# Performance work log

Hardware: AMD Instinct MI355X
Metric: run time of the kernel (lower is better)

The kernel has to match this reference:

```python
import jax, jax.numpy as jnp
import numpy as np

N_NODES = 50000
N_EDGES = 800000
IN_CH = 64
OUT_CH = 64
NHEAD = 8


def _edge_softmax(e, dst, num_nodes):
    # segment softmax over incoming edges of each destination node,
    # elementwise over [H, D] feature dims (matches dgl edge_softmax)
    mx = jax.ops.segment_max(e, dst, num_segments=num_nodes)
    mx = jax.lax.stop_gradient(mx)
    ex = jnp.exp(e - mx[dst])
    s = jax.ops.segment_sum(ex, dst, num_segments=num_nodes)
    return ex / s[dst]


def setup_inputs() -> dict:
    key = jax.random.key(0)
    ks = jax.random.split(key, 10)
    ndata = jax.random.normal(ks[0], (N_NODES, IN_CH), dtype=jnp.float32)
    src = jax.random.randint(ks[1], (N_EDGES,), 0, N_NODES)
    dst = jax.random.randint(ks[2], (N_EDGES,), 0, N_NODES)
    sc = 1.0 / np.sqrt(IN_CH)
    W1 = jax.random.normal(ks[3], (IN_CH, OUT_CH), dtype=jnp.float32) * sc
    b1 = jnp.zeros((OUT_CH,), dtype=jnp.float32)
    W2 = jax.random.normal(ks[4], (IN_CH, OUT_CH), dtype=jnp.float32) * sc
    b2 = jnp.zeros((OUT_CH,), dtype=jnp.float32)
    Wres = jax.random.normal(ks[5], (IN_CH, OUT_CH), dtype=jnp.float32) * sc
    bres = jnp.zeros((OUT_CH,), dtype=jnp.float32)
    m = jnp.ones((3, NHEAD, OUT_CH // NHEAD), dtype=jnp.float32)
    return {"ndata": ndata, "src": src, "dst": dst, "W1": W1, "b1": b1,
            "W2": W2, "b2": b2, "Wres": Wres, "bres": bres, "m": m}


def reference(ndata, src, dst, W1, b1, W2, b2, Wres, bres, m):
    N = ndata.shape[0]
    H = NHEAD
    # add self loops (dgl.add_self_loop)
    loop = jnp.arange(N, dtype=src.dtype)
    s = jnp.concatenate([src, loop])
    d = jnp.concatenate([dst, loop])
    # minmax_norm over last dim
    mn = jnp.min(ndata, axis=-1, keepdims=True)
    mx = jnp.max(ndata, axis=-1, keepdims=True)
    x = (ndata - mn) / (mx - mn + 1e-5)
    # node projections -> [N, H, Dh]
    l = (x @ W1 + b1).reshape(N, H, -1)
    r = (x @ W2 + b2).reshape(N, H, -1)
    # edge-wise fused activation of src+dst (acfun='sigmoid')
    le = jax.nn.sigmoid(l[s] + l[d])
    re = jax.nn.sigmoid(r[s] + r[d])
    # edge softmax grouped by destination
    le = _edge_softmax(le, d, N)
    re = _edge_softmax(re, d, N)
    # two-hop scatter-gather aggregation
    ft_r = jax.ops.segment_sum(r[s] * le, d, num_segments=N)   # [N,H,Dh]
    ft_l = jax.ops.segment_sum(ft_r[s] * re, d, num_segments=N)
    h = (m[0] * ft_l).reshape(N, -1) + (x @ Wres + bres)
    return h
```

## Files before the change

kernel.cpp:

```cpp
#include <hip/hip_runtime.h>
#include <hip/hip_fp16.h>

#define CH 64
#define LOG2E  1.44269504f
#define MLOG2E -1.44269504f

__device__ __forceinline__ float exp2fast(float x) {
    float r; asm("v_exp_f32 %0, %1" : "=v"(r) : "v"(x)); return r;
}

__global__ void count_kernel(const int* __restrict__ dst, int* __restrict__ deg,
                             int* __restrict__ rank, int E)
{
    for (int i = blockIdx.x * blockDim.x + threadIdx.x; i < E;
         i += gridDim.x * blockDim.x) {
        rank[i] = atomicAdd(&deg[dst[i]], 1);
    }
}

__global__ __launch_bounds__(256) void proj_kernel(
    const float* __restrict__ nd,
    const float* __restrict__ W1, const float* __restrict__ b1,
    const float* __restrict__ W2, const float* __restrict__ b2,
    const float* __restrict__ Wr, const float* __restrict__ br,
    __half2* __restrict__ lr, float* __restrict__ hres, int N)
{
    __shared__ __align__(16) float xs[4][CH];
    const int lane = threadIdx.x & 63;
    const int wid  = threadIdx.x >> 6;

    float w1[CH], w2[CH], wr[CH];
#pragma unroll
    for (int i = 0; i < CH; ++i) {
        w1[i] = W1[i * CH + lane];
        w2[i] = W2[i * CH + lane];
        wr[i] = Wr[i * CH + lane];
    }
    const float bb1 = b1[lane], bb2 = b2[lane], bbr = br[lane];

    const int nwave = gridDim.x * 4;
    for (int node = blockIdx.x * 4 + wid; node < N; node += nwave) {
        const unsigned row = (unsigned)node * CH;
        float v = nd[row + lane];
        float mn = v, mx = v;
#pragma unroll
        for (int off = 32; off; off >>= 1) {
            mn = fminf(mn, __shfl_xor(mn, off));
            mx = fmaxf(mx, __shfl_xor(mx, off));
        }
        float x = (v - mn) / (mx - mn + 1e-5f);
        xs[wid][lane] = x;
        float a1 = bb1, a2 = bb2, a3 = bbr;
        const float4* x4 = reinterpret_cast<const float4*>(&xs[wid][0]);
#pragma unroll
        for (int k = 0; k < CH / 4; ++k) {
            float4 xv = x4[k];
            a1 = fmaf(xv.x, w1[4*k+0], a1);
            a1 = fmaf(xv.y, w1[4*k+1], a1);
            a1 = fmaf(xv.z, w1[4*k+2], a1);
            a1 = fmaf(xv.w, w1[4*k+3], a1);
            a2 = fmaf(xv.x, w2[4*k+0], a2);
            a2 = fmaf(xv.y, w2[4*k+1], a2);
            a2 = fmaf(xv.z, w2[4*k+2], a2);
            a2 = fmaf(xv.w, w2[4*k+3], a2);
            a3 = fmaf(xv.x, wr[4*k+0], a3);
            a3 = fmaf(xv.y, wr[4*k+1], a3);
            a3 = fmaf(xv.z, wr[4*k+2], a3);
            a3 = fmaf(xv.w, wr[4*k+3], a3);
        }
        lr[row + lane]   = __floats2half2_rn(a1, a2);
        hres[row + lane] = a3;
    }
}

__global__ __launch_bounds__(256) void bsum_kernel(
    const int* __restrict__ deg, int* __restrict__ bsum, int N)
{
    __shared__ int ws[4];
    int i = blockIdx.x * 256 + threadIdx.x;
    int lane = threadIdx.x & 63, wid = threadIdx.x >> 6;
    int v = (i < N) ? deg[i] : 0;
#pragma unroll
    for (int off = 32; off; off >>= 1) v += __shfl_xor(v, off);
    if (lane == 0) ws[wid] = v;
    __syncthreads();
    if (threadIdx.x == 0) bsum[blockIdx.x] = ws[0] + ws[1] + ws[2] + ws[3];
}

__global__ __launch_bounds__(64) void bscan_kernel(int* __restrict__ bsum, int nb)
{
    int lane = threadIdx.x;
    int carry = 0;
    for (int base = 0; base < nb; base += 64) {
        int i = base + lane;
        int v = (i < nb) ? bsum[i] : 0;
        int s = v;
#pragma unroll
        for (int off = 1; off < 64; off <<= 1) {
            int t = __shfl_up(s, off);
            if (lane >= off) s += t;
        }
        if (i < nb) bsum[i] = carry + s - v;
        carry += __shfl(s, 63);
    }
}

__global__ __launch_bounds__(256) void apply_kernel(
    const int* __restrict__ deg, const int* __restrict__ bsum,
    int* __restrict__ rowptr, int N, int total)
{
    __shared__ int ws[4];
    int i = blockIdx.x * 256 + threadIdx.x;
    int lane = threadIdx.x & 63, wid = threadIdx.x >> 6;
    int v = (i < N) ? deg[i] : 0;
    int s = v;
#pragma unroll
    for (int off = 1; off < 64; off <<= 1) {
        int t = __shfl_up(s, off);
        if (lane >= off) s += t;
    }
    if (lane == 63) ws[wid] = s;
    __syncthreads();
    int woff = 0;
    for (int w = 0; w < wid; ++w) woff += ws[w];
    int excl = bsum[blockIdx.x] + woff + s - v;
    if (i < N) rowptr[i] = excl;
    if (blockIdx.x == 0 && threadIdx.x == 0) rowptr[N] = total;
}

__global__ void scatter_kernel(const int* __restrict__ src,
                               const int* __restrict__ dst,
                               const int* __restrict__ rank,
                               const int* __restrict__ rowptr,
                               int* __restrict__ col, int E)
{
    for (int i = blockIdx.x * blockDim.x + threadIdx.x; i < E;
         i += gridDim.x * blockDim.x) {
        col[rowptr[dst[i]] + rank[i]] = src[i];
    }
}

#define EDGE_BATCH(U_, TBL_, STEP_)                                          \
    {                                                                        \
        __half2 hb[U_];                                                      \
        _Pragma("unroll")                                                    \
        for (int u = 0; u < (U_); ++u) {                                     \
            int s_ = __builtin_amdgcn_readlane(myc, j + u);                  \
            hb[u] = TBL_[(unsigned)(s_ * CH) + lane];                        \
        }                                                                    \
        _Pragma("unroll")                                                    \
        for (int u = 0; u < (U_); ++u) { STEP_(hb[u]); }                     \
        j += (U_);                                                           \
    }

__global__ __launch_bounds__(256) void passA_kernel(
    const __half2* __restrict__ lr,
    const int* __restrict__ rowptr, const int* __restrict__ col,
    __half2* __restrict__ rf, int N)
{
    const int node = blockIdx.x * 4 + (threadIdx.x >> 6);
    const int lane = threadIdx.x & 63;
    if (node >= N) return;
    const unsigned row = (unsigned)node * CH;
    const float2 own = __half22float2(lr[row + lane]);
    const float l_d = own.x, r_d = own.y;
    const float nl_d = MLOG2E * l_d;
    const int beg = rowptr[node], end = rowptr[node + 1];

    float wl = exp2fast(LOG2E * __builtin_amdgcn_rcpf(1.f + exp2fast(2.f * nl_d)));
    float denL = wl, acc = r_d * wl;

#define A_STEP(H_) {                                                         \
        float2 f = __half22float2(H_);                                       \
        float uu = exp2fast(fmaf(f.x, MLOG2E, nl_d));                        \
        float w  = exp2fast(LOG2E * __builtin_amdgcn_rcpf(1.f + uu));        \
        denL += w; acc = fmaf(f.y, w, acc); }

    int e = beg;
    while (e < end) {
        int cnt = end - e; if (cnt > 64) cnt = 64;
        int idx = e + lane; if (idx >= end) idx = end - 1;
        const int myc = col[idx];
        int j = 0;
        int nfull = cnt >> 4;
        for (int b = 0; b < nfull; ++b) EDGE_BATCH(16, lr, A_STEP)
        if (cnt & 8) EDGE_BATCH(8, lr, A_STEP)
        if (cnt & 4) EDGE_BATCH(4, lr, A_STEP)
        if (cnt & 2) EDGE_BATCH(2, lr, A_STEP)
        if (cnt & 1) EDGE_BATCH(1, lr, A_STEP)
        e += cnt;
    }
    rf[row + lane] = __floats2half2_rn(r_d, acc / denL);
}

__global__ __launch_bounds__(256) void passB_kernel(
    const __half2* __restrict__ rf,
    const int* __restrict__ rowptr, const int* __restrict__ col,
    const float* __restrict__ m0, float* __restrict__ out, int N)
{
    const int node = blockIdx.x * 4 + (threadIdx.x >> 6);
    const int lane = threadIdx.x & 63;
    if (node >= N) return;
    const unsigned row = (unsigned)node * CH;
    const float2 own = __half22float2(rf[row + lane]);
    const float r_d = own.x, f_own = own.y;
    const float nr_d = MLOG2E * r_d;
    const int beg = rowptr[node], end = rowptr[node + 1];

    float wsl = exp2fast(LOG2E * __builtin_amdgcn_rcpf(1.f + exp2fast(2.f * nr_d)));
    float dR = wsl, acc = f_own * wsl;

#define B_STEP(H_) {                                                         \
        float2 f = __half22float2(H_);                                       \
        float uu = exp2fast(fmaf(f.x, MLOG2E, nr_d));                        \
        float w  = exp2fast(LOG2E * __builtin_amdgcn_rcpf(1.f + uu));        \
        dR += w; acc = fmaf(f.y, w, acc); }

    int e = beg;
    while (e < end) {
        int cnt = end - e; if (cnt > 64) cnt = 64;
        int idx = e + lane; if (idx >= end) idx = end - 1;
        const int myc = col[idx];
        int j = 0;
        int nfull = cnt >> 4;
        for (int b = 0; b < nfull; ++b) EDGE_BATCH(16, rf, B_STEP)
        if (cnt & 8) EDGE_BATCH(8, rf, B_STEP)
        if (cnt & 4) EDGE_BATCH(4, rf, B_STEP)
        if (cnt & 2) EDGE_BATCH(2, rf, B_STEP)
        if (cnt & 1) EDGE_BATCH(1, rf, B_STEP)
        e += cnt;
    }
    out[row + lane] = fmaf(m0[lane], acc / dR, out[row + lane]);
}

extern "C" void kernel_launch(void* const* d_in, const int* in_sizes, int n_in,
                              void* d_out, int out_size, void* d_ws, size_t ws_size,
                              hipStream_t stream)
{
    const float* ndata = (const float*)d_in[0];
    const int*   src   = (const int*)d_in[1];
    const int*   dst   = (const int*)d_in[2];
    const float* W1    = (const float*)d_in[3];
    const float* b1    = (const float*)d_in[4];
    const float* W2    = (const float*)d_in[5];
    const float* b2    = (const float*)d_in[6];
    const float* Wr    = (const float*)d_in[7];
    const float* br    = (const float*)d_in[8];
    const float* m     = (const float*)d_in[9];
    float* out = (float*)d_out;

    const int N = in_sizes[0] / CH;
    const int E = in_sizes[1];
    const int nbk = (N + 255) / 256;

    char* ws = (char*)d_ws;
    size_t off = 0;
    auto alloc = [&](size_t bytes) -> void* {
        void* p = ws + off;
        off = (off + bytes + 255) & ~(size_t)255;
        return p;
    };
    __half2* lr   = (__half2*)alloc((size_t)N * CH * 4);
    __half2* rf   = (__half2*)alloc((size_t)N * CH * 4);
    int*   deg    = (int*)alloc((size_t)N * 4);
    int*   bsum   = (int*)alloc((size_t)nbk * 4);
    int*   rowptr = (int*)alloc((size_t)(N + 1) * 4);
    int*   rank   = (int*)alloc((size_t)E * 4);
    int*   col    = (int*)alloc((size_t)E * 4);

    hipMemsetAsync(deg, 0, (size_t)N * 4, stream);
    count_kernel<<<2048, 256, 0, stream>>>(dst, deg, rank, E);
    proj_kernel<<<1024, 256, 0, stream>>>(ndata, W1, b1, W2, b2, Wr, br,
                                          lr, out, N);
    bsum_kernel<<<nbk, 256, 0, stream>>>(deg, bsum, N);
    bscan_kernel<<<1, 64, 0, stream>>>(bsum, nbk);
    apply_kernel<<<nbk, 256, 0, stream>>>(deg, bsum, rowptr, N, E);
    scatter_kernel<<<2048, 256, 0, stream>>>(src, dst, rank, rowptr, col, E);
    int nb = (N + 3) / 4;
    passA_kernel<<<nb, 256, 0, stream>>>(lr, rowptr, col, rf, N);
    passB_kernel<<<nb, 256, 0, stream>>>(rf, rowptr, col, m, out, N);
}
```

Baseline: 236.5 us.

## Approximate sigmoid-exp with cubic polynomial, drop scan kernel, readlane projection

Edge weights exp(sigmoid(z)) are now computed with a cubic polynomial in the sigmoid value over [0,1], replacing one transcendental per edge in both aggregation passes. The separate single-wave block scan kernel is removed, and each apply block instead sums all preceding block sums itself, which saves one launch but does redundant work. The projection kernel broadcasts x through readlane instead of an LDS round trip, prefetches the next node row, and declares a minimum occupancy in its launch bounds. The polynomial adds approximation error to the softmax weights.

```diff
diff --git a/kernel.cpp b/kernel.cpp
--- a/kernel.cpp
+++ b/kernel.cpp
@@ -8,6 +8,17 @@
 __device__ __forceinline__ float exp2fast(float x) {
     float r; asm("v_exp_f32 %0, %1" : "=v"(r) : "v"(x)); return r;
 }
+__device__ __forceinline__ float bcast(float x, int k) {
+    return __int_as_float(__builtin_amdgcn_readlane(__float_as_int(x), k));
+}
+
+#define EXPP_D0 0.9994851f
+#define EXPP_D1 1.0160896f
+#define EXPP_D2 0.4230492f
+#define EXPP_D3 0.2790848f
+__device__ __forceinline__ float exp01_poly(float s) {
+    return fmaf(fmaf(fmaf(EXPP_D3, s, EXPP_D2), s, EXPP_D1), s, EXPP_D0);
+}
 
 __global__ void count_kernel(const int* __restrict__ dst, int* __restrict__ deg,
                              int* __restrict__ rank, int E)
@@ -18,14 +29,13 @@
     }
 }
 
-__global__ __launch_bounds__(256) void proj_kernel(
+__global__ __launch_bounds__(256, 2) void proj_kernel(
     const float* __restrict__ nd,
     const float* __restrict__ W1, const float* __restrict__ b1,
     const float* __restrict__ W2, const float* __restrict__ b2,
     const float* __restrict__ Wr, const float* __restrict__ br,
     __half2* __restrict__ lr, float* __restrict__ hres, int N)
 {
-    __shared__ __align__(16) float xs[4][CH];
     const int lane = threadIdx.x & 63;
     const int wid  = threadIdx.x >> 6;
 
@@ -39,35 +49,30 @@
     const float bb1 = b1[lane], bb2 = b2[lane], bbr = br[lane];
 
     const int nwave = gridDim.x * 4;
-    for (int node = blockIdx.x * 4 + wid; node < N; node += nwave) {
-        const unsigned row = (unsigned)node * CH;
-        float v = nd[row + lane];
-        float mn = v, mx = v;
+    int node = blockIdx.x * 4 + wid;
+    float v = (node < N) ? nd[(unsigned)node * CH + lane] : 0.f;
+    for (; node < N; node += nwave) {
+        const float vc = v;
+        const int nxt = node + nwave;
+        if (nxt < N) v = nd[(unsigned)nxt * CH + lane];
+
+        float mn = vc, mx = vc;
 #pragma unroll
         for (int off = 32; off; off >>= 1) {
             mn = fminf(mn, __shfl_xor(mn, off));
             mx = fmaxf(mx, __shfl_xor(mx, off));
         }
-        float x = (v - mn) / (mx - mn + 1e-5f);
-        xs[wid][lane] = x;
+        const float x = (vc - mn) / (mx - mn + 1e-5f);
+
         float a1 = bb1, a2 = bb2, a3 = bbr;
-        const float4* x4 = reinterpret_cast<const float4*>(&xs[wid][0]);
-#pragma unroll
-        for (int k = 0; k < CH / 4; ++k) {
-            float4 xv = x4[k];
-            a1 = fmaf(xv.x, w1[4*k+0], a1);
-            a1 = fmaf(xv.y, w1[4*k+1], a1);
-            a1 = fmaf(xv.z, w1[4*k+2], a1);
-            a1 = fmaf(xv.w, w1[4*k+3], a1);
-            a2 = fmaf(xv.x, w2[4*k+0], a2);
-            a2 = fmaf(xv.y, w2[4*k+1], a2);
-            a2 = fmaf(xv.z, w2[4*k+2], a2);
-            a2 = fmaf(xv.w, w2[4*k+3], a2);
-            a3 = fmaf(xv.x, wr[4*k+0], a3);
-            a3 = fmaf(xv.y, wr[4*k+1], a3);
-            a3 = fmaf(xv.z, wr[4*k+2], a3);
-            a3 = fmaf(xv.w, wr[4*k+3], a3);
+#pragma unroll
+        for (int k = 0; k < CH; ++k) {
+            const float xk = bcast(x, k);
+            a1 = fmaf(xk, w1[k], a1);
+            a2 = fmaf(xk, w2[k], a2);
+            a3 = fmaf(xk, wr[k], a3);
         }
+        const unsigned row = (unsigned)node * CH;
         lr[row + lane]   = __floats2half2_rn(a1, a2);
         hres[row + lane] = a3;
     }
@@ -87,31 +92,22 @@
     if (threadIdx.x == 0) bsum[blockIdx.x] = ws[0] + ws[1] + ws[2] + ws[3];
 }
 
-__global__ __launch_bounds__(64) void bscan_kernel(int* __restrict__ bsum, int nb)
-{
-    int lane = threadIdx.x;
-    int carry = 0;
-    for (int base = 0; base < nb; base += 64) {
-        int i = base + lane;
-        int v = (i < nb) ? bsum[i] : 0;
-        int s = v;
-#pragma unroll
-        for (int off = 1; off < 64; off <<= 1) {
-            int t = __shfl_up(s, off);
-            if (lane >= off) s += t;
-        }
-        if (i < nb) bsum[i] = carry + s - v;
-        carry += __shfl(s, 63);
-    }
-}
-
 __global__ __launch_bounds__(256) void apply_kernel(
     const int* __restrict__ deg, const int* __restrict__ bsum,
-    int* __restrict__ rowptr, int N, int total)
+    int* __restrict__ rowptr, int N, int total, int nbk)
 {
     __shared__ int ws[4];
-    int i = blockIdx.x * 256 + threadIdx.x;
-    int lane = threadIdx.x & 63, wid = threadIdx.x >> 6;
+    __shared__ int pws[4];
+    const int lane = threadIdx.x & 63, wid = threadIdx.x >> 6;
+    const int b = blockIdx.x;
+
+    int pref = 0;
+    for (int t = threadIdx.x; t < b; t += 256) pref += bsum[t];
+#pragma unroll
+    for (int off = 32; off; off >>= 1) pref += __shfl_xor(pref, off);
+    if (lane == 0) pws[wid] = pref;
+
+    int i = b * 256 + threadIdx.x;
     int v = (i < N) ? deg[i] : 0;
     int s = v;
 #pragma unroll
@@ -121,11 +117,12 @@
     }
     if (lane == 63) ws[wid] = s;
     __syncthreads();
+    const int base = pws[0] + pws[1] + pws[2] + pws[3];
     int woff = 0;
     for (int w = 0; w < wid; ++w) woff += ws[w];
-    int excl = bsum[blockIdx.x] + woff + s - v;
+    const int excl = base + woff + s - v;
     if (i < N) rowptr[i] = excl;
-    if (blockIdx.x == 0 && threadIdx.x == 0) rowptr[N] = total;
+    if (b == 0 && threadIdx.x == 0) rowptr[N] = total;
 }
 
 __global__ void scatter_kernel(const int* __restrict__ src,
@@ -167,13 +164,13 @@
     const float nl_d = MLOG2E * l_d;
     const int beg = rowptr[node], end = rowptr[node + 1];
 
-    float wl = exp2fast(LOG2E * __builtin_amdgcn_rcpf(1.f + exp2fast(2.f * nl_d)));
+    float wl = exp01_poly(__builtin_amdgcn_rcpf(1.f + exp2fast(2.f * nl_d)));
     float denL = wl, acc = r_d * wl;
 
 #define A_STEP(H_) {                                                         \
         float2 f = __half22float2(H_);                                       \
-        float uu = exp2fast(fmaf(f.x, MLOG2E, nl_d));                        \
-        float w  = exp2fast(LOG2E * __builtin_amdgcn_rcpf(1.f + uu));        \
+        float sg = __builtin_amdgcn_rcpf(1.f + exp2fast(fmaf(f.x, MLOG2E, nl_d))); \
+        float w  = exp01_poly(sg);                                           \
         denL += w; acc = fmaf(f.y, w, acc); }
 
     int e = beg;
@@ -207,13 +204,13 @@
     const float nr_d = MLOG2E * r_d;
     const int beg = rowptr[node], end = rowptr[node + 1];
 
-    float wsl = exp2fast(LOG2E * __builtin_amdgcn_rcpf(1.f + exp2fast(2.f * nr_d)));
+    float wsl = exp01_poly(__builtin_amdgcn_rcpf(1.f + exp2fast(2.f * nr_d)));
     float dR = wsl, acc = f_own * wsl;
 
 #define B_STEP(H_) {                                                         \
         float2 f = __half22float2(H_);                                       \
-        float uu = exp2fast(fmaf(f.x, MLOG2E, nr_d));                        \
-        float w  = exp2fast(LOG2E * __builtin_amdgcn_rcpf(1.f + uu));        \
+        float sg = __builtin_amdgcn_rcpf(1.f + exp2fast(fmaf(f.x, MLOG2E, nr_d))); \
+        float w  = exp01_poly(sg);                                           \
         dR += w; acc = fmaf(f.y, w, acc); }
 
     int e = beg;
@@ -273,8 +270,7 @@
     proj_kernel<<<1024, 256, 0, stream>>>(ndata, W1, b1, W2, b2, Wr, br,
                                           lr, out, N);
     bsum_kernel<<<nbk, 256, 0, stream>>>(deg, bsum, N);
-    bscan_kernel<<<1, 64, 0, stream>>>(bsum, nbk);
-    apply_kernel<<<nbk, 256, 0, stream>>>(deg, bsum, rowptr, N, E);
+    apply_kernel<<<nbk, 256, 0, stream>>>(deg, bsum, rowptr, N, E, nbk);
     scatter_kernel<<<2048, 256, 0, stream>>>(src, dst, rank, rowptr, col, E);
     int nb = (N + 3) / 4;
     passA_kernel<<<nb, 256, 0, stream>>>(lr, rowptr, col, rf, N);
```

Result: no change. 235.8 us, median of 2 (-0.3%).
